# Kernel optimization log

Hardware: AMD Instinct MI355X
Metric: run time of the kernel (lower is better)

## Reference

```python
import jax, jax.numpy as jnp
import numpy as np

N_NODES = 100000
N_EDGES = 600000
IN_DIM, HID, OUT = 6, 128, 1
EPS = 1e-5


def _glorot(key, shape):
    fan_in, fan_out = shape[1], shape[0]
    lim = jnp.sqrt(6.0 / (fan_in + fan_out))
    return jax.random.uniform(key, shape, jnp.float32, -lim, lim)


def setup_inputs() -> dict:
    key = jax.random.key(0)
    ks = jax.random.split(key, 16)
    x = jax.random.normal(ks[0], (N_NODES, IN_DIM), jnp.float32)
    edge_index = jax.random.randint(ks[1], (2, N_EDGES), 0, N_NODES, jnp.int64)
    return {
        "x": x,
        "edge_index": edge_index,
        # SAGEConv layer 0: 6 -> 128 (lin_l acts on aggregated neighbors, lin_r on root)
        "w_l0": _glorot(ks[2], (HID, IN_DIM)), "b_l0": jnp.zeros((HID,), jnp.float32),
        "w_r0": _glorot(ks[3], (HID, IN_DIM)),
        "bn_g0": jnp.ones((HID,), jnp.float32), "bn_b0": jnp.zeros((HID,), jnp.float32),
        # SAGEConv layer 1: 128 -> 128
        "w_l1": _glorot(ks[4], (HID, HID)), "b_l1": jnp.zeros((HID,), jnp.float32),
        "w_r1": _glorot(ks[5], (HID, HID)),
        "bn_g1": jnp.ones((HID,), jnp.float32), "bn_b1": jnp.zeros((HID,), jnp.float32),
        # SAGEConv layer 2: 128 -> 1
        "w_l2": _glorot(ks[6], (OUT, HID)), "b_l2": jnp.zeros((OUT,), jnp.float32),
        "w_r2": _glorot(ks[7], (OUT, HID)),
    }


def _sage_conv(x, src, dst, inv_deg, w_l, b_l, w_r):
    # mean aggregation of source-node features into destination nodes
    agg = jax.ops.segment_sum(x[src], dst, num_segments=N_NODES)  # [N, d]
    mean_nb = agg * inv_deg[:, None]
    return mean_nb @ w_l.T + b_l + x @ w_r.T


def _batch_norm(x, gamma, beta):
    mu = jnp.mean(x, axis=0)
    var = jnp.mean(jnp.square(x - mu), axis=0)  # biased, as torch BN training
    return (x - mu) * jax.lax.rsqrt(var + EPS) * gamma + beta


def reference(x, edge_index, w_l0, b_l0, w_r0, bn_g0, bn_b0,
              w_l1, b_l1, w_r1, bn_g1, bn_b1, w_l2, b_l2, w_r2):
    src, dst = edge_index[0], edge_index[1]
    deg = jax.ops.segment_sum(jnp.ones_like(dst, dtype=x.dtype), dst,
                              num_segments=N_NODES)
    inv_deg = 1.0 / jnp.maximum(deg, 1.0)

    h = _sage_conv(x, src, dst, inv_deg, w_l0, b_l0, w_r0)
    h = jax.nn.relu(_batch_norm(h, bn_g0, bn_b0))  # dropout = identity (eval)

    h = _sage_conv(h, src, dst, inv_deg, w_l1, b_l1, w_r1)
    h = jax.nn.relu(_batch_norm(h, bn_g1, bn_b1))

    h = _sage_conv(h, src, dst, inv_deg, w_l2, b_l2, w_r2)
    return jax.nn.sigmoid(h).squeeze(-1)  # [N]
```

## Files before the change

kernel.cpp:

```cpp
#include <hip/hip_runtime.h>
#include <math.h>

#define HID 128
#define INDIM 6

typedef float4 f4;
typedef __attribute__((ext_vector_type(8))) short short8;
typedef __attribute__((ext_vector_type(4))) float f32x4;

static __device__ inline unsigned short f2bf(float f) {
    union { float f; unsigned int u; } v; v.f = f;
    unsigned int r = v.u + 0x7fffu + ((v.u >> 16) & 1u);
    return (unsigned short)(r >> 16);
}
static __device__ inline float bf2f_lo(unsigned int u) {
    union { unsigned int u; float f; } v; v.u = u << 16; return v.f;
}
static __device__ inline float bf2f_hi(unsigned int u) {
    union { unsigned int u; float f; } v; v.u = u & 0xffff0000u; return v.f;
}

__global__ void k_zero2(int* a, int na, int* b, int nb) {
    int i = blockIdx.x * blockDim.x + threadIdx.x;
    if (i < na) a[i] = 0;
    if (i < nb) b[i] = 0;
}

__global__ void k_deg(const int* dst, int* deg, int* rank, int E) {
    int e = blockIdx.x * blockDim.x + threadIdx.x;
    if (e < E) rank[e] = atomicAdd(&deg[dst[e]], 1);
}

__global__ void k_scan_partial(const int* __restrict__ deg, int* __restrict__ partial, int N) {
    __shared__ int lds[256];
    int t = threadIdx.x;
    int base = blockIdx.x * 1024 + t * 4;
    int s = 0;
    if (base + 4 <= N) {
        int4 v = *(const int4*)&deg[base];
        s = v.x + v.y + v.z + v.w;
    } else {
        for (int i = 0; i < 4; i++) if (base + i < N) s += deg[base + i];
    }
    lds[t] = s;
    __syncthreads();
    for (int off = 128; off > 0; off >>= 1) {
        if (t < off) lds[t] += lds[t + off];
        __syncthreads();
    }
    if (t == 0) partial[blockIdx.x] = lds[0];
}

__global__ void k_scan_tops(int* partial, int nb) {
    __shared__ int lds[1024];
    int t = threadIdx.x;
    lds[t] = (t < nb) ? partial[t] : 0;
    __syncthreads();
    for (int off = 1; off < 1024; off <<= 1) {
        int v = (t >= off) ? lds[t - off] : 0;
        __syncthreads();
        lds[t] += v;
        __syncthreads();
    }
    if (t < nb) partial[t] = (t == 0) ? 0 : lds[t - 1];
}

__global__ void k_scan_write(const int* __restrict__ deg, const int* __restrict__ partial,
                             int* __restrict__ rowptr, int N, int E) {
    __shared__ int lds[256];
    int t = threadIdx.x;
    int base = blockIdx.x * 1024 + t * 4;
    int v0 = 0, v1 = 0, v2 = 0, v3 = 0;
    if (base + 4 <= N) {
        int4 v = *(const int4*)&deg[base];
        v0 = v.x; v1 = v.y; v2 = v.z; v3 = v.w;
    } else {
        if (base + 0 < N) v0 = deg[base + 0];
        if (base + 1 < N) v1 = deg[base + 1];
        if (base + 2 < N) v2 = deg[base + 2];
        if (base + 3 < N) v3 = deg[base + 3];
    }
    lds[t] = v0 + v1 + v2 + v3;
    __syncthreads();
    for (int off = 1; off < 256; off <<= 1) {
        int v = (t >= off) ? lds[t - off] : 0;
        __syncthreads();
        lds[t] += v;
        __syncthreads();
    }
    int run = partial[blockIdx.x] + ((t == 0) ? 0 : lds[t - 1]);
    if (base + 0 < N) rowptr[base + 0] = run; run += v0;
    if (base + 1 < N) rowptr[base + 1] = run; run += v1;
    if (base + 2 < N) rowptr[base + 2] = run; run += v2;
    if (base + 3 < N) rowptr[base + 3] = run; run += v3;
    if (blockIdx.x == 0 && t == 0) rowptr[N] = E;
}

__global__ void k_fill(const int* ei, const int* rank, const int* rowptr, int* csr, int E) {
    int e = blockIdx.x * blockDim.x + threadIdx.x;
    if (e < E) {
        int d = ei[E + e];
        csr[rowptr[d] + rank[e]] = ei[e];
    }
}

__global__ void k_invdeg(const int* deg, float* invd, int N) {
    int i = blockIdx.x * blockDim.x + threadIdx.x;
    if (i < N) invd[i] = 1.0f / (float)max(deg[i], 1);
}

__global__ void k_prepw(const float* __restrict__ wl, const float* __restrict__ wr,
                        unsigned short* __restrict__ wcat) {
    int i = blockIdx.x * 256 + threadIdx.x;
    int o = i >> 8, k = i & 255;
    float v = (k < 128) ? wl[o * 128 + k] : wr[o * 128 + k - 128];
    wcat[i] = f2bf(v);
}

__global__ __launch_bounds__(256) void k_layer0(
        const float* __restrict__ x, const int* __restrict__ rowptr,
        const int* __restrict__ csr, const float* __restrict__ invd,
        const float* __restrict__ wl, const float* __restrict__ bl,
        const float* __restrict__ wr, float* __restrict__ out,
        float* __restrict__ sum8, float* __restrict__ sq8, int N) {
    __shared__ float wlds[1600];
    __shared__ float blds[136];
    __shared__ float mx[32][8];
    __shared__ float xr[32][8];
    __shared__ float ps[4][128];
    __shared__ float pq[4][128];
    int t = threadIdx.x;
    for (int idx = t; idx < 1536; idx += 256) {
        int half = idx >= 768 ? 1 : 0;
        int lin = idx - half * 768;
        int o = lin / 6, i = lin - o * 6;
        float v = half ? wr[lin] : wl[lin];
        wlds[half * 800 + o * 6 + i + (o >> 4) * 2] = v;
    }
    if (t < 128) blds[t + (t >> 4)] = bl[t];
    int nl = t >> 3, f = t & 7;
    int n = blockIdx.x * 32 + nl;
    bool valid = n < N;
    if (f < 6) {
        float mean = 0.f, xv = 0.f;
        if (valid) {
            int s = rowptr[n], e = rowptr[n + 1];
            float acc = 0.f;
            int i = s;
            for (; i + 4 <= e; i += 4) {
                int i0 = csr[i], i1 = csr[i + 1], i2 = csr[i + 2], i3 = csr[i + 3];
                float a0 = x[i0 * 6 + f], a1 = x[i1 * 6 + f];
                float a2 = x[i2 * 6 + f], a3 = x[i3 * 6 + f];
                acc += (a0 + a1) + (a2 + a3);
            }
            for (; i < e; i++) acc += x[csr[i] * 6 + f];
            mean = acc * invd[n];
            xv = x[n * 6 + f];
        }
        mx[nl][f] = mean;
        xr[nl][f] = xv;
    }
    __syncthreads();
    float m0 = mx[nl][0], m1 = mx[nl][1], m2 = mx[nl][2];
    float m3 = mx[nl][3], m4 = mx[nl][4], m5 = mx[nl][5];
    float r0 = xr[nl][0], r1 = xr[nl][1], r2 = xr[nl][2];
    float r3 = xr[nl][3], r4 = xr[nl][4], r5 = xr[nl][5];
    const float* wA = wlds;
    const float* wB = wlds + 800;
    float sk[16], qk[16];
#pragma unroll
    for (int k4 = 0; k4 < 4; k4++) {
        f4 hv;
        float* hp = &hv.x;
#pragma unroll
        for (int j = 0; j < 4; j++) {
            int k = k4 * 4 + j;
            int o = f * 16 + k;
            int wb = 98 * f + 6 * k;
            float h = blds[o + f];
            h += m0 * wA[wb] + m1 * wA[wb + 1] + m2 * wA[wb + 2]
               + m3 * wA[wb + 3] + m4 * wA[wb + 4] + m5 * wA[wb + 5];
            h += r0 * wB[wb] + r1 * wB[wb + 1] + r2 * wB[wb + 2]
               + r3 * wB[wb + 3] + r4 * wB[wb + 4] + r5 * wB[wb + 5];
            hp[j] = h;
            float hs = valid ? h : 0.f;
            sk[k] = hs;
            qk[k] = hs * hs;
        }
        if (valid) *(f4*)&out[(size_t)n * HID + f * 16 + k4 * 4] = hv;
    }
    int wv = t >> 6, lane = t & 63;
#pragma unroll
    for (int k = 0; k < 16; k++) {
        float s = sk[k], q = qk[k];
        s += __shfl_xor(s, 8, 64);  q += __shfl_xor(q, 8, 64);
        s += __shfl_xor(s, 16, 64); q += __shfl_xor(q, 16, 64);
        s += __shfl_xor(s, 32, 64); q += __shfl_xor(q, 32, 64);
        if (lane < 8) { ps[wv][lane * 16 + k] = s; pq[wv][lane * 16 + k] = q; }
    }
    __syncthreads();
    if (t < 128) {
        float S = ps[0][t] + ps[1][t] + ps[2][t] + ps[3][t];
        float Q = pq[0][t] + pq[1][t] + pq[2][t] + pq[3][t];
        int slot = (blockIdx.x & 7) * 128 + t;
        atomicAdd(&sum8[slot], S);
        atomicAdd(&sq8[slot], Q);
    }
}

__global__ void k_bnfin8(const float* sum8, const float* sq8, const float* g, const float* b,
                         float* scale, float* shift, float invN) {
    int t = threadIdx.x;
    float s = 0.f, q = 0.f;
    for (int c = 0; c < 8; c++) { s += sum8[c * 128 + t]; q += sq8[c * 128 + t]; }
    float mu  = s * invN;
    float var = q * invN - mu * mu;
    float sc  = g[t] * rsqrtf(var + 1e-5f);
    scale[t] = sc;
    shift[t] = b[t] - mu * sc;
}

__global__ void k_bnapply(const float* __restrict__ h, const float* __restrict__ scale,
                          const float* __restrict__ shift, unsigned short* __restrict__ out,
                          int total8) {
    int i = blockIdx.x * blockDim.x + threadIdx.x;
    int stride = gridDim.x * blockDim.x;
    for (; i < total8; i += stride) {
        int f8 = (i & 15) * 8;
        f4 v0 = ((const f4*)h)[i * 2];
        f4 v1 = ((const f4*)h)[i * 2 + 1];
        f4 sc0v = *(const f4*)&scale[f8];
        f4 sc1v = *(const f4*)&scale[f8 + 4];
        f4 sh0v = *(const f4*)&shift[f8];
        f4 sh1v = *(const f4*)&shift[f8 + 4];
        unsigned short pk[8];
        pk[0] = f2bf(fmaxf(0.f, fmaf(v0.x, sc0v.x, sh0v.x)));
        pk[1] = f2bf(fmaxf(0.f, fmaf(v0.y, sc0v.y, sh0v.y)));
        pk[2] = f2bf(fmaxf(0.f, fmaf(v0.z, sc0v.z, sh0v.z)));
        pk[3] = f2bf(fmaxf(0.f, fmaf(v0.w, sc0v.w, sh0v.w)));
        pk[4] = f2bf(fmaxf(0.f, fmaf(v1.x, sc1v.x, sh1v.x)));
        pk[5] = f2bf(fmaxf(0.f, fmaf(v1.y, sc1v.y, sh1v.y)));
        pk[6] = f2bf(fmaxf(0.f, fmaf(v1.z, sc1v.z, sh1v.z)));
        pk[7] = f2bf(fmaxf(0.f, fmaf(v1.w, sc1v.w, sh1v.w)));
        *(uint4*)&out[(size_t)i * 8] = *(const uint4*)pk;
    }
}

__global__ void k_agg_bf(const unsigned short* __restrict__ hb, const int* __restrict__ rowptr,
                         const int* __restrict__ csr, const float* __restrict__ invd,
                         unsigned short* __restrict__ out, int N) {
    int t = threadIdx.x;
    int w = t >> 6, lid = t & 63;
    int half = lid >> 5, l32 = lid & 31;
    int n = blockIdx.x * 8 + w * 2 + half;
    if (n >= N) return;
    int s = rowptr[n], e = rowptr[n + 1];
    const uint2* hb64 = (const uint2*)hb;
    float ax0 = 0.f, ay0 = 0.f, ax1 = 0.f, ay1 = 0.f;
    int i = s;
    for (; i + 4 <= e; i += 4) {
        int i0 = csr[i], i1 = csr[i + 1], i2 = csr[i + 2], i3 = csr[i + 3];
        uint2 u0 = hb64[(size_t)i0 * 32 + l32];
        uint2 u1 = hb64[(size_t)i1 * 32 + l32];
        uint2 u2 = hb64[(size_t)i2 * 32 + l32];
        uint2 u3 = hb64[(size_t)i3 * 32 + l32];
        ax0 += (bf2f_lo(u0.x) + bf2f_lo(u1.x)) + (bf2f_lo(u2.x) + bf2f_lo(u3.x));
        ay0 += (bf2f_hi(u0.x) + bf2f_hi(u1.x)) + (bf2f_hi(u2.x) + bf2f_hi(u3.x));
        ax1 += (bf2f_lo(u0.y) + bf2f_lo(u1.y)) + (bf2f_lo(u2.y) + bf2f_lo(u3.y));
        ay1 += (bf2f_hi(u0.y) + bf2f_hi(u1.y)) + (bf2f_hi(u2.y) + bf2f_hi(u3.y));
    }
    for (; i < e; i++) {
        uint2 u = hb64[(size_t)csr[i] * 32 + l32];
        ax0 += bf2f_lo(u.x); ay0 += bf2f_hi(u.x);
        ax1 += bf2f_lo(u.y); ay1 += bf2f_hi(u.y);
    }
    float id = invd[n];
    uint2 r;
    r.x = (unsigned int)f2bf(ax0 * id) | ((unsigned int)f2bf(ay0 * id) << 16);
    r.y = (unsigned int)f2bf(ax1 * id) | ((unsigned int)f2bf(ay1 * id) << 16);
    ((uint2*)out)[(size_t)n * 32 + l32] = r;
}

__global__ __launch_bounds__(256) void k_gemm(
        const unsigned short* __restrict__ Bm, const unsigned short* __restrict__ Ar,
        const unsigned short* __restrict__ wcat, const float* __restrict__ bias,
        float* __restrict__ sum8, float* __restrict__ sq8,
        float* __restrict__ C, int N) {
    __shared__ __align__(16) unsigned short As[128][40];
    __shared__ __align__(16) unsigned short Ws[128][40];
    __shared__ float lds_s[2][128];
    __shared__ float lds_q[2][128];
    int t = threadIdx.x;
    int wave = t >> 6, lane = t & 63;
    int wr = wave >> 1, wc = wave & 1;
    int row0 = blockIdx.x * 128;
    int r = t >> 1, half = t & 1;

    f32x4 acc[4][4];
#pragma unroll
    for (int m = 0; m < 4; m++)
#pragma unroll
        for (int n = 0; n < 4; n++) acc[m][n] = (f32x4)(0.f);

    for (int chunk = 0; chunk < 8; chunk++) {
        int kb = chunk * 32;
        int srow = row0 + r;
        int c0 = (chunk & 3) * 32 + half * 16;
        const unsigned short* src = (chunk < 4) ? Bm : Ar;
        if (srow < N) {
            const unsigned short* p = src + (size_t)srow * HID + c0;
            *(uint4*)&As[r][half * 16]     = *(const uint4*)(p);
            *(uint4*)&As[r][half * 16 + 8] = *(const uint4*)(p + 8);
        } else {
            uint4 z = make_uint4(0, 0, 0, 0);
            *(uint4*)&As[r][half * 16]     = z;
            *(uint4*)&As[r][half * 16 + 8] = z;
        }
        const unsigned short* wp = wcat + r * 256 + kb + half * 16;
        *(uint4*)&Ws[r][half * 16]     = *(const uint4*)(wp + 0);
        *(uint4*)&Ws[r][half * 16 + 8] = *(const uint4*)(wp + 8);
        __syncthreads();

        int lrow = lane & 15, koff = (lane >> 4) * 8;
        short8 af[4], bfr[4];
#pragma unroll
        for (int m = 0; m < 4; m++)
            af[m] = *(const short8*)&As[wr * 64 + m * 16 + lrow][koff];
#pragma unroll
        for (int n = 0; n < 4; n++)
            bfr[n] = *(const short8*)&Ws[wc * 64 + n * 16 + lrow][koff];
#pragma unroll
        for (int m = 0; m < 4; m++)
#pragma unroll
            for (int n = 0; n < 4; n++)
                acc[m][n] = __builtin_amdgcn_mfma_f32_16x16x32_bf16(af[m], bfr[n], acc[m][n], 0, 0, 0);
        __syncthreads();
    }

    int cl = lane & 15, rq = (lane >> 4) * 4;
    float cs[4], cq[4];
#pragma unroll
    for (int n = 0; n < 4; n++) {
        int col = wc * 64 + n * 16 + cl;
        float bn = bias[col];
        float s = 0.f, q = 0.f;
#pragma unroll
        for (int m = 0; m < 4; m++) {
#pragma unroll
            for (int reg = 0; reg < 4; reg++) {
                int row = row0 + wr * 64 + m * 16 + rq + reg;
                float v = acc[m][n][reg] + bn;
                if (row < N) {
                    C[(size_t)row * HID + col] = v;
                    s += v;
                    q += v * v;
                }
            }
        }
        cs[n] = s; cq[n] = q;
    }
#pragma unroll
    for (int n = 0; n < 4; n++) {
        float s = cs[n], q = cq[n];
        s += __shfl_xor(s, 16, 64); q += __shfl_xor(q, 16, 64);
        s += __shfl_xor(s, 32, 64); q += __shfl_xor(q, 32, 64);
        if (lane < 16) {
            int col = wc * 64 + n * 16 + cl;
            lds_s[wr][col] = s;
            lds_q[wr][col] = q;
        }
    }
    __syncthreads();
    if (t < 128) {
        float S = lds_s[0][t] + lds_s[1][t];
        float Q = lds_q[0][t] + lds_q[1][t];
        int slot = (blockIdx.x & 7) * 128 + t;
        atomicAdd(&sum8[slot], S);
        atomicAdd(&sq8[slot], Q);
    }
}

__global__ void k_dots(const float* __restrict__ h, const float* __restrict__ scale,
                       const float* __restrict__ shift, const float* __restrict__ wl2,
                       const float* __restrict__ wr2, float* __restrict__ s_arr,
                       float* __restrict__ r_arr, int N) {
    int w = threadIdx.x >> 6, lid = threadIdx.x & 63;
    int n = blockIdx.x * 4 + w;
    if (n >= N) return;
    float2 v  = *(const float2*)&h[(size_t)n * HID + lid * 2];
    float2 sc = *(const float2*)&scale[lid * 2];
    float2 sh = *(const float2*)&shift[lid * 2];
    float y0 = fmaxf(0.f, fmaf(v.x, sc.x, sh.x));
    float y1 = fmaxf(0.f, fmaf(v.y, sc.y, sh.y));
    float2 wl = *(const float2*)&wl2[lid * 2];
    float2 wrv = *(const float2*)&wr2[lid * 2];
    float ps = y0 * wl.x + y1 * wl.y;
    float pr = y0 * wrv.x + y1 * wrv.y;
#pragma unroll
    for (int off = 32; off > 0; off >>= 1) {
        ps += __shfl_down(ps, off, 64);
        pr += __shfl_down(pr, off, 64);
    }
    if (lid == 0) { s_arr[n] = ps; r_arr[n] = pr; }
}

__global__ void k_final2(const float* __restrict__ s_arr, const float* __restrict__ r_arr,
                         const int* __restrict__ rowptr, const int* __restrict__ csr,
                         const float* __restrict__ invd, const float* __restrict__ bl2,
                         float* __restrict__ out, int N) {
    int n = blockIdx.x * blockDim.x + threadIdx.x;
    if (n >= N) return;
    int s = rowptr[n], e = rowptr[n + 1];
    float a = 0.f;
    int i = s;
    for (; i + 4 <= e; i += 4) {
        float a0 = s_arr[csr[i]],     a1 = s_arr[csr[i + 1]];
        float a2 = s_arr[csr[i + 2]], a3 = s_arr[csr[i + 3]];
        a += (a0 + a1) + (a2 + a3);
    }
    for (; i < e; i++) a += s_arr[csr[i]];
    float p = a * invd[n] + r_arr[n] + bl2[0];
    out[n] = 1.f / (1.f + expf(-p));
}

extern "C" void kernel_launch(void* const* d_in, const int* in_sizes, int n_in,
                              void* d_out, int out_size, void* d_ws, size_t ws_size,
                              hipStream_t stream) {
    const float* x   = (const float*)d_in[0];
    const int*   ei  = (const int*)d_in[1];
    const float* wl0 = (const float*)d_in[2];
    const float* bl0 = (const float*)d_in[3];
    const float* wr0 = (const float*)d_in[4];
    const float* g0  = (const float*)d_in[5];
    const float* be0 = (const float*)d_in[6];
    const float* wl1 = (const float*)d_in[7];
    const float* bl1 = (const float*)d_in[8];
    const float* wr1 = (const float*)d_in[9];
    const float* g1  = (const float*)d_in[10];
    const float* be1 = (const float*)d_in[11];
    const float* wl2 = (const float*)d_in[12];
    const float* bl2 = (const float*)d_in[13];
    const float* wr2 = (const float*)d_in[14];
    float* outp = (float*)d_out;

    int N = in_sizes[0] / INDIM;
    int E = in_sizes[1] / 2;

    char* ws = (char*)d_ws;
    size_t off = 0;
    auto alloc = [&](size_t bytes) { size_t o = off; off = (off + bytes + 255) & ~(size_t)255; return o; };
    int*   degi   = (int*)(ws + alloc((size_t)N * 4));
    int*   rank   = (int*)(ws + alloc((size_t)E * 4));
    int*   rowptr = (int*)(ws + alloc((size_t)(N + 1) * 4));
    int*   csr    = (int*)(ws + alloc((size_t)E * 4));
    float* invd   = (float*)(ws + alloc((size_t)N * 4));
    int*   partial= (int*)(ws + alloc(1024 * 4));
    float* bnbuf  = (float*)(ws + alloc(5120 * 4));
    unsigned short* wcat = (unsigned short*)(ws + alloc(128 * 256 * 2));
    float* sarr   = (float*)(ws + alloc((size_t)N * 4));
    float* rarr   = (float*)(ws + alloc((size_t)N * 4));
    float* sum0_8 = bnbuf;
    float* sq0_8  = bnbuf + 1024;
    float* sum1_8 = bnbuf + 2048;
    float* sq1_8  = bnbuf + 3072;
    float* sc0 = bnbuf + 4096, *sh0 = bnbuf + 4224;
    float* sc1 = bnbuf + 4352, *sh1 = bnbuf + 4480;
    float* bufA = (float*)(ws + alloc((size_t)N * HID * 4));
    float* bufB = (float*)(ws + alloc((size_t)N * HID * 4));
    unsigned short* bufC = (unsigned short*)(ws + alloc((size_t)N * HID * 2));
    unsigned short* bufD = (unsigned short*)bufA;

    float invN = 1.0f / (float)N;
    int gE = (E + 255) / 256;
    int gN = (N + 255) / 256;
    int gW = (N + 3) / 4;
    int gA = (N + 7) / 8;
    int gL = (N + 31) / 32;
    int gS = (N + 127) / 128;
    int nbScan = (N + 1023) / 1024;
    int total8 = N * (HID / 8);

    k_zero2<<<gN, 256, 0, stream>>>(degi, N, (int*)bnbuf, 4096);

    k_prepw<<<128, 256, 0, stream>>>(wl1, wr1, wcat);

    k_deg<<<gE, 256, 0, stream>>>(ei + E, degi, rank, E);
    k_scan_partial<<<nbScan, 256, 0, stream>>>(degi, partial, N);
    k_scan_tops<<<1, 1024, 0, stream>>>(partial, nbScan);
    k_scan_write<<<nbScan, 256, 0, stream>>>(degi, partial, rowptr, N, E);
    k_fill<<<gE, 256, 0, stream>>>(ei, rank, rowptr, csr, E);
    k_invdeg<<<gN, 256, 0, stream>>>(degi, invd, N);

    k_layer0<<<gL, 256, 0, stream>>>(x, rowptr, csr, invd, wl0, bl0, wr0, bufA,
                                     sum0_8, sq0_8, N);
    k_bnfin8<<<1, 128, 0, stream>>>(sum0_8, sq0_8, g0, be0, sc0, sh0, invN);

    k_bnapply<<<2048, 256, 0, stream>>>(bufA, sc0, sh0, bufC, total8);

    k_agg_bf<<<gA, 256, 0, stream>>>(bufC, rowptr, csr, invd, bufD, N);
    k_gemm<<<gS, 256, 0, stream>>>(bufD, bufC, wcat, bl1, sum1_8, sq1_8, bufB, N);
    k_bnfin8<<<1, 128, 0, stream>>>(sum1_8, sq1_8, g1, be1, sc1, sh1, invN);

    k_dots<<<gW, 256, 0, stream>>>(bufB, sc1, sh1, wl2, wr2, sarr, rarr, N);
    k_final2<<<gN, 256, 0, stream>>>(sarr, rarr, rowptr, csr, invd, bl2, outp, N);
}
```

Measured before the change: 208.6 us.

## Recompute layer-0 linear after BN stats instead of storing fp32 hidden

Layer 0 is split into a stats pass and an apply pass. The stats pass saves only the 6-dim neighbour mean per node and accumulates the BN sums. The apply pass recomputes the small 6-to-128 linear transform, then applies BN and ReLU and writes bf16 directly. This removes the write and re-read of the 128-wide fp32 intermediate and drops the separate BN-apply kernel, in exchange for duplicated weight staging and arithmetic plus a small extra mean buffer.

Measured after the change: 234.6 us. 12.5% more time.

```diff
diff --git a/kernel.cpp b/kernel.cpp
--- a/kernel.cpp
+++ b/kernel.cpp
@@ -117,11 +117,11 @@
     wcat[i] = f2bf(v);
 }
 
-__global__ __launch_bounds__(256) void k_layer0(
+__global__ __launch_bounds__(256) void k_l0stats(
         const float* __restrict__ x, const int* __restrict__ rowptr,
         const int* __restrict__ csr, const float* __restrict__ invd,
         const float* __restrict__ wl, const float* __restrict__ bl,
-        const float* __restrict__ wr, float* __restrict__ out,
+        const float* __restrict__ wr, float* __restrict__ mean6,
         float* __restrict__ sum8, float* __restrict__ sq8, int N) {
     __shared__ float wlds[1600];
     __shared__ float blds[136];
@@ -156,6 +156,7 @@
             for (; i < e; i++) acc += x[csr[i] * 6 + f];
             mean = acc * invd[n];
             xv = x[n * 6 + f];
+            mean6[n * 6 + f] = mean;
         }
         mx[nl][f] = mean;
         xr[nl][f] = xv;
@@ -170,8 +171,6 @@
     float sk[16], qk[16];
 #pragma unroll
     for (int k4 = 0; k4 < 4; k4++) {
-        f4 hv;
-        float* hp = &hv.x;
 #pragma unroll
         for (int j = 0; j < 4; j++) {
             int k = k4 * 4 + j;
@@ -182,12 +181,10 @@
                + m3 * wA[wb + 3] + m4 * wA[wb + 4] + m5 * wA[wb + 5];
             h += r0 * wB[wb] + r1 * wB[wb + 1] + r2 * wB[wb + 2]
                + r3 * wB[wb + 3] + r4 * wB[wb + 4] + r5 * wB[wb + 5];
-            hp[j] = h;
             float hs = valid ? h : 0.f;
             sk[k] = hs;
             qk[k] = hs * hs;
         }
-        if (valid) *(f4*)&out[(size_t)n * HID + f * 16 + k4 * 4] = hv;
     }
     int wv = t >> 6, lane = t & 63;
 #pragma unroll
@@ -206,6 +203,66 @@
         atomicAdd(&sum8[slot], S);
         atomicAdd(&sq8[slot], Q);
     }
+}
+
+__global__ __launch_bounds__(256) void k_l0apply(
+        const float* __restrict__ x, const float* __restrict__ mean6,
+        const float* __restrict__ wl, const float* __restrict__ bl,
+        const float* __restrict__ wr, const float* __restrict__ scale,
+        const float* __restrict__ shift, unsigned short* __restrict__ out, int N) {
+    __shared__ float wlds[1600];
+    __shared__ float blds[136];
+    __shared__ float sclds[136];
+    __shared__ float shlds[136];
+    __shared__ float mx[32][8];
+    __shared__ float xr[32][8];
+    int t = threadIdx.x;
+    for (int idx = t; idx < 1536; idx += 256) {
+        int half = idx >= 768 ? 1 : 0;
+        int lin = idx - half * 768;
+        int o = lin / 6, i = lin - o * 6;
+        float v = half ? wr[lin] : wl[lin];
+        wlds[half * 800 + o * 6 + i + (o >> 4) * 2] = v;
+    }
+    if (t < 128) {
+        blds[t + (t >> 4)]  = bl[t];
+        sclds[t + (t >> 4)] = scale[t];
+        shlds[t + (t >> 4)] = shift[t];
+    }
+    int nl = t >> 3, f = t & 7;
+    int n = blockIdx.x * 32 + nl;
+    bool valid = n < N;
+    if (f < 6) {
+        mx[nl][f] = valid ? mean6[n * 6 + f] : 0.f;
+        xr[nl][f] = valid ? x[n * 6 + f] : 0.f;
+    }
+    __syncthreads();
+    if (!valid) return;
+    float m0 = mx[nl][0], m1 = mx[nl][1], m2 = mx[nl][2];
+    float m3 = mx[nl][3], m4 = mx[nl][4], m5 = mx[nl][5];
+    float r0 = xr[nl][0], r1 = xr[nl][1], r2 = xr[nl][2];
+    float r3 = xr[nl][3], r4 = xr[nl][4], r5 = xr[nl][5];
+    const float* wA = wlds;
+    const float* wB = wlds + 800;
+    unsigned short pk[16];
+#pragma unroll
+    for (int k4 = 0; k4 < 4; k4++) {
+#pragma unroll
+        for (int j = 0; j < 4; j++) {
+            int k = k4 * 4 + j;
+            int o = f * 16 + k;
+            int wb = 98 * f + 6 * k;
+            float h = blds[o + f];
+            h += m0 * wA[wb] + m1 * wA[wb + 1] + m2 * wA[wb + 2]
+               + m3 * wA[wb + 3] + m4 * wA[wb + 4] + m5 * wA[wb + 5];
+            h += r0 * wB[wb] + r1 * wB[wb + 1] + r2 * wB[wb + 2]
+               + r3 * wB[wb + 3] + r4 * wB[wb + 4] + r5 * wB[wb + 5];
+            pk[k] = f2bf(fmaxf(0.f, fmaf(h, sclds[o + f], shlds[o + f])));
+        }
+    }
+    unsigned short* dst = out + (size_t)n * HID + f * 16;
+    *(uint4*)(dst)     = *(const uint4*)&pk[0];
+    *(uint4*)(dst + 8) = *(const uint4*)&pk[8];
 }
 
 __global__ void k_bnfin8(const float* sum8, const float* sq8, const float* g, const float* b,
@@ -218,32 +275,6 @@
     float sc  = g[t] * rsqrtf(var + 1e-5f);
     scale[t] = sc;
     shift[t] = b[t] - mu * sc;
-}
-
-__global__ void k_bnapply(const float* __restrict__ h, const float* __restrict__ scale,
-                          const float* __restrict__ shift, unsigned short* __restrict__ out,
-                          int total8) {
-    int i = blockIdx.x * blockDim.x + threadIdx.x;
-    int stride = gridDim.x * blockDim.x;
-    for (; i < total8; i += stride) {
-        int f8 = (i & 15) * 8;
-        f4 v0 = ((const f4*)h)[i * 2];
-        f4 v1 = ((const f4*)h)[i * 2 + 1];
-        f4 sc0v = *(const f4*)&scale[f8];
-        f4 sc1v = *(const f4*)&scale[f8 + 4];
-        f4 sh0v = *(const f4*)&shift[f8];
-        f4 sh1v = *(const f4*)&shift[f8 + 4];
-        unsigned short pk[8];
-        pk[0] = f2bf(fmaxf(0.f, fmaf(v0.x, sc0v.x, sh0v.x)));
-        pk[1] = f2bf(fmaxf(0.f, fmaf(v0.y, sc0v.y, sh0v.y)));
-        pk[2] = f2bf(fmaxf(0.f, fmaf(v0.z, sc0v.z, sh0v.z)));
-        pk[3] = f2bf(fmaxf(0.f, fmaf(v0.w, sc0v.w, sh0v.w)));
-        pk[4] = f2bf(fmaxf(0.f, fmaf(v1.x, sc1v.x, sh1v.x)));
-        pk[5] = f2bf(fmaxf(0.f, fmaf(v1.y, sc1v.y, sh1v.y)));
-        pk[6] = f2bf(fmaxf(0.f, fmaf(v1.z, sc1v.z, sh1v.z)));
-        pk[7] = f2bf(fmaxf(0.f, fmaf(v1.w, sc1v.w, sh1v.w)));
-        *(uint4*)&out[(size_t)i * 8] = *(const uint4*)pk;
-    }
 }
 
 __global__ void k_agg_bf(const unsigned short* __restrict__ hb, const int* __restrict__ rowptr,
@@ -459,16 +490,16 @@
     unsigned short* wcat = (unsigned short*)(ws + alloc(128 * 256 * 2));
     float* sarr   = (float*)(ws + alloc((size_t)N * 4));
     float* rarr   = (float*)(ws + alloc((size_t)N * 4));
+    float* mean6  = (float*)(ws + alloc((size_t)N * 6 * 4));
     float* sum0_8 = bnbuf;
     float* sq0_8  = bnbuf + 1024;
     float* sum1_8 = bnbuf + 2048;
     float* sq1_8  = bnbuf + 3072;
     float* sc0 = bnbuf + 4096, *sh0 = bnbuf + 4224;
     float* sc1 = bnbuf + 4352, *sh1 = bnbuf + 4480;
-    float* bufA = (float*)(ws + alloc((size_t)N * HID * 4));
     float* bufB = (float*)(ws + alloc((size_t)N * HID * 4));
     unsigned short* bufC = (unsigned short*)(ws + alloc((size_t)N * HID * 2));
-    unsigned short* bufD = (unsigned short*)bufA;
+    unsigned short* bufD = (unsigned short*)(ws + alloc((size_t)N * HID * 2));
 
     float invN = 1.0f / (float)N;
     int gE = (E + 255) / 256;
@@ -478,7 +509,6 @@
     int gL = (N + 31) / 32;
     int gS = (N + 127) / 128;
     int nbScan = (N + 1023) / 1024;
-    int total8 = N * (HID / 8);
 
     k_zero2<<<gN, 256, 0, stream>>>(degi, N, (int*)bnbuf, 4096);
 
@@ -491,11 +521,11 @@
     k_fill<<<gE, 256, 0, stream>>>(ei, rank, rowptr, csr, E);
     k_invdeg<<<gN, 256, 0, stream>>>(degi, invd, N);
 
-    k_layer0<<<gL, 256, 0, stream>>>(x, rowptr, csr, invd, wl0, bl0, wr0, bufA,
-                                     sum0_8, sq0_8, N);
+    k_l0stats<<<gL, 256, 0, stream>>>(x, rowptr, csr, invd, wl0, bl0, wr0, mean6,
+                                      sum0_8, sq0_8, N);
     k_bnfin8<<<1, 128, 0, stream>>>(sum0_8, sq0_8, g0, be0, sc0, sh0, invN);
 
-    k_bnapply<<<2048, 256, 0, stream>>>(bufA, sc0, sh0, bufC, total8);
+    k_l0apply<<<gL, 256, 0, stream>>>(x, mean6, wl0, bl0, wr0, sc0, sh0, bufC, N);
 
     k_agg_bf<<<gA, 256, 0, stream>>>(bufC, rowptr, csr, invd, bufD, N);
     k_gemm<<<gS, 256, 0, stream>>>(bufD, bufC, wcat, bl1, sum1_8, sq1_8, bufB, N);
```
